# Kernel tuning notes

Hardware: AMD Instinct MI355X
Metric: run time of the kernel (lower is better)

## Reference

```python
import jax, jax.numpy as jnp
import numpy as np
import math

B, S, D = 16, 256, 1024   # batch, seq (= s_model), d_model
HP, HC = 16, 8
DK, SK = D // HP, S // HC
EPS = 1e-6


def setup_inputs() -> dict:
    key = jax.random.key(0)
    ks = jax.random.split(key, 3)
    x = jax.random.normal(ks[0], (B, S, D), dtype=jnp.float32)
    Wp = jax.random.normal(ks[1], (3, D, D), dtype=jnp.float32) * 0.02  # (in,out)
    bp = jnp.zeros((3, D), dtype=jnp.float32)
    Wc = jax.random.normal(ks[2], (4, S, S), dtype=jnp.float32) * 0.02  # (in,out)
    bc = jnp.zeros((4, S), dtype=jnp.float32)
    a_p = jnp.ones((D,), dtype=jnp.float32)
    b_p = jnp.zeros((D,), dtype=jnp.float32)
    a_c = jnp.ones((S,), dtype=jnp.float32)
    b_c = jnp.zeros((S,), dtype=jnp.float32)
    return {"x": x, "Wp": Wp, "bp": bp, "Wc": Wc, "bc": bc,
            "a_p": a_p, "b_p": b_p, "a_c": a_c, "b_c": b_c}


def _std(x, axis):
    # torch .std(): unbiased (ddof=1)
    return jnp.std(x, axis=axis, keepdims=True, ddof=1)


def _attn(q, k, v):
    # q,k,v: [B, H, T, dk]; dropout is identity (eval)
    scores = jnp.einsum('bhtd,bhsd->bhts', q, k) / math.sqrt(q.shape[-1])
    p = jax.nn.softmax(scores, axis=-1)
    return jnp.einsum('bhts,bhsd->bhtd', p, v)


def reference(x, Wp, bp, Wc, bc, a_p, b_p, a_c, b_c):
    nb = x.shape[0]
    # ---- LayerNorm over channels (norm_p) ----
    mean = jnp.mean(x, axis=-1, keepdims=True)
    xp = a_p * (x - mean) / (_std(x, -1) + EPS) + b_p            # [B,S,D]
    # ---- positional attention over sequence ----
    qkv = jnp.einsum('bsd,nde->nbse', xp, Wp) + bp[:, None, None, :]
    q, k, v = [t.reshape(nb, S, HP, DK).transpose(0, 2, 1, 3) for t in qkv]
    xp = _attn(q, k, v).transpose(0, 2, 1, 3).reshape(nb, S, D)  # [B,S,D]
    # ---- LayerNorm_C: stats over sequence dim, affine indexed by seq ----
    mean_c = jnp.mean(xp, axis=-2, keepdims=True)                # [B,1,D]
    xc = a_c[:, None] * (xp - mean_c) / (_std(xp, -2) + EPS) + b_c[:, None]
    # ---- channel attention: channels are tokens, head dim SK ----
    xt = xc.transpose(0, 2, 1)                                    # [B,D,S]
    qkvc = jnp.einsum('bds,nse->nbde', xt, Wc[:3]) + bc[:3, None, None, :]
    qc, kc, vc = [t.reshape(nb, D, HC, SK).transpose(0, 2, 1, 3) for t in qkvc]
    xcatt = _attn(qc, kc, vc).transpose(0, 2, 1, 3).reshape(nb, D, S)  # [B,D,S]
    out = jnp.einsum('bds,se->bde', xcatt, Wc[3]) + bc[3]         # [B,D,S]
    return out.transpose(0, 2, 1)                                  # [B,S,D]
```

## Files before the change

kernel.cpp:

```cpp
#include <hip/hip_runtime.h>
#include <hip/hip_bf16.h>
#include <math.h>

#define B_ 16
#define S_ 256
#define D_ 1024
#define HP_ 16
#define DK_ 64
#define HC_ 8
#define SK_ 32
#define EPS_ 1e-6f

#define ALPHA_P 0.42466089973135876f
#define ALPHA_C 0.50500991942f

typedef __attribute__((ext_vector_type(8))) short short8v;
typedef __attribute__((ext_vector_type(4))) float f32x4;

__device__ __forceinline__ float bf2f(unsigned short h) {
    return __uint_as_float((unsigned)h << 16);
}
__device__ __forceinline__ ushort2 f2bf2(float a, float b) {
    __hip_bfloat162 h = __float22bfloat162_rn(make_float2(a, b));
    union { __hip_bfloat162 h2; ushort2 u2; } cv;
    cv.h2 = h;
    return cv.u2;
}
__device__ __forceinline__ float exp2_fast(float x) {
    float r;
    asm("v_exp_f32 %0, %1\n\ts_nop 0" : "=v"(r) : "v"(x));
    return r;
}
__device__ __forceinline__ void ldlds16(const unsigned short* g, unsigned short* l) {
    const unsigned int* gp = reinterpret_cast<const unsigned int*>(g);
    auto* lp = reinterpret_cast<__attribute__((address_space(3))) unsigned int*>(
        reinterpret_cast<uintptr_t>(l));
    __builtin_amdgcn_global_load_lds(gp, lp, 16, 0, 0);
}

__global__ __launch_bounds__(256) void k1_ln_p(
    const float* __restrict__ x, const float* __restrict__ a_p,
    const float* __restrict__ b_p, unsigned short* __restrict__ xh,
    unsigned short* __restrict__ xl)
{
    const int row = blockIdx.x;
    const float4* xr = (const float4*)(x + (size_t)row * D_);
    const int tid = threadIdx.x;
    float4 v = xr[tid];
    float s  = v.x + v.y + v.z + v.w;
    float sq = v.x*v.x + v.y*v.y + v.z*v.z + v.w*v.w;
    #pragma unroll
    for (int off = 32; off > 0; off >>= 1) {
        s  += __shfl_down(s, off);
        sq += __shfl_down(sq, off);
    }
    __shared__ float red[8];
    const int wid = tid >> 6, lane = tid & 63;
    if (lane == 0) { red[wid] = s; red[4 + wid] = sq; }
    __syncthreads();
    if (tid == 0) {
        float S0 = red[0] + red[1] + red[2] + red[3];
        float Q0 = red[4] + red[5] + red[6] + red[7];
        float mean = S0 / (float)D_;
        float var  = fmaxf((Q0 - (float)D_ * mean * mean) / (float)(D_ - 1), 0.0f);
        red[0] = mean;
        red[1] = 1.0f / (sqrtf(var) + EPS_);
    }
    __syncthreads();
    const float mean = red[0], inv = red[1];
    float4 a = ((const float4*)a_p)[tid];
    float4 b = ((const float4*)b_p)[tid];
    float o0 = a.x * (v.x - mean) * inv + b.x;
    float o1 = a.y * (v.y - mean) * inv + b.y;
    float o2 = a.z * (v.z - mean) * inv + b.z;
    float o3 = a.w * (v.w - mean) * inv + b.w;
    ushort2 h01 = f2bf2(o0, o1), h23 = f2bf2(o2, o3);
    ushort2 l01 = f2bf2(o0 - bf2f(h01.x), o1 - bf2f(h01.y));
    ushort2 l23 = f2bf2(o2 - bf2f(h23.x), o3 - bf2f(h23.y));
    ushort4 hv, lv;
    hv.x = h01.x; hv.y = h01.y; hv.z = h23.x; hv.w = h23.y;
    lv.x = l01.x; lv.y = l01.y; lv.z = l23.x; lv.w = l23.y;
    *(ushort4*)&xh[(size_t)row * D_ + tid*4] = hv;
    *(ushort4*)&xl[(size_t)row * D_ + tid*4] = lv;
}

__global__ __launch_bounds__(256) void tsplit(
    const float* __restrict__ W, unsigned short* __restrict__ Th,
    unsigned short* __restrict__ Tl, int K, int N)
{
    const int z = blockIdx.z;
    W  += (size_t)z * K * N;
    Th += (size_t)z * K * N;
    Tl += (size_t)z * K * N;
    const int k0 = blockIdx.x * 64, n0 = blockIdx.y * 64;
    __shared__ float tile[64][65];
    const int ix = threadIdx.x & 63, iy = threadIdx.x >> 6;
    #pragma unroll
    for (int u = 0; u < 16; u++) {
        const int kk = iy*16 + u;
        tile[kk][ix] = W[(size_t)(k0+kk)*N + n0 + ix];
    }
    __syncthreads();
    #pragma unroll
    for (int u = 0; u < 16; u += 2) {
        const int nn0 = iy*16 + u, nn1 = nn0 + 1;
        const float v0 = tile[ix][nn0], v1 = tile[ix][nn1];
        ushort2 h2 = f2bf2(v0, v1);
        ushort2 l2 = f2bf2(v0 - bf2f(h2.x), v1 - bf2f(h2.y));
        Th[(size_t)(n0+nn0)*K + k0 + ix] = h2.x;
        Th[(size_t)(n0+nn1)*K + k0 + ix] = h2.y;
        Tl[(size_t)(n0+nn0)*K + k0 + ix] = l2.x;
        Tl[(size_t)(n0+nn1)*K + k0 + ix] = l2.y;
    }
}

template<int OUTMODE>
__global__ __launch_bounds__(256) void mm_mfma(
    const unsigned short* __restrict__ Ah, const unsigned short* __restrict__ Al,
    const unsigned short* __restrict__ Bh, const unsigned short* __restrict__ Bl,
    const float* __restrict__ bias, void* __restrict__ Cout1,
    void* __restrict__ Cout2,
    int M, int N, int K, long sB, long sBias, long sC, long loff, int TB,
    float alpha, int zsplit, int zobase, int lognx)
{
    const int nwg = gridDim.x * gridDim.y * gridDim.z;
    const int chunk = nwg >> 3;
    const int flat = blockIdx.x + gridDim.x * (blockIdx.y + gridDim.y * blockIdx.z);
    const int logical = (flat & 7) * chunk + (flat >> 3);
    const int bz  = logical >> 8;
    const int rem = logical & 255;
    const int bx  = rem & ((1 << lognx) - 1);
    const int by  = rem >> lognx;
    const int zeff = bz + zobase;
    Bh   += (size_t)bz * sB;
    Bl   += (size_t)bz * sB;
    bias += (size_t)zeff * sBias;
    const int n0 = bx * 128, m0 = by * 128;
    __shared__ __align__(16) unsigned short Ash[2][128*32], Als[2][128*32];
    __shared__ __align__(16) unsigned short Bsh[2][128*32], Bls[2][128*32];
    const int tid = threadIdx.x;
    const int wave = tid >> 6, lane = tid & 63;
    const int wm = wave & 1, wn = wave >> 1;
    const int lrow = lane & 15, quad = lane >> 4;
    size_t gaOff[2], gbOff[2];
    int cb[2];
    #pragma unroll
    for (int j = 0; j < 2; j++) {
        const int p = wave*128 + j*64 + lane;
        const int row = p >> 2;
        const int cc = (p & 3) ^ ((row >> 1) & 3);
        gaOff[j] = (size_t)(m0 + row) * K + cc*8;
        gbOff[j] = (size_t)(n0 + row) * K + cc*8;
        cb[j] = (wave*128 + j*64) * 8;
    }
    int aFr[4], bFr[4];
    #pragma unroll
    for (int i = 0; i < 4; i++) {
        const int ra = wm*64 + i*16 + lrow;
        aFr[i] = ((ra << 2) | (quad ^ ((ra >> 1) & 3))) * 8;
        const int rb = wn*64 + i*16 + lrow;
        bFr[i] = ((rb << 2) | (quad ^ ((rb >> 1) & 3))) * 8;
    }
    f32x4 acc[4][4];
    #pragma unroll
    for (int j = 0; j < 4; j++) {
        const float bv = bias[n0 + wn*64 + j*16 + lrow];
        #pragma unroll
        for (int i = 0; i < 4; i++) {
            acc[i][j][0] = bv; acc[i][j][1] = bv; acc[i][j][2] = bv; acc[i][j][3] = bv;
        }
    }
    #pragma unroll
    for (int j = 0; j < 2; j++) {
        ldlds16(Ah + gaOff[j], &Ash[0][cb[j]]);
        ldlds16(Al + gaOff[j], &Als[0][cb[j]]);
        ldlds16(Bh + gbOff[j], &Bsh[0][cb[j]]);
        ldlds16(Bl + gbOff[j], &Bls[0][cb[j]]);
    }
    const int NT = K >> 5;
    for (int kt = 0; kt < NT; kt++) {
        const int cur = kt & 1;
        asm volatile("s_waitcnt vmcnt(0)" ::: "memory");
        asm volatile("s_barrier" ::: "memory");
        if (kt + 1 < NT) {
            const int kk = (kt + 1) * 32;
            #pragma unroll
            for (int j = 0; j < 2; j++) {
                ldlds16(Ah + gaOff[j] + kk, &Ash[cur^1][cb[j]]);
                ldlds16(Al + gaOff[j] + kk, &Als[cur^1][cb[j]]);
                ldlds16(Bh + gbOff[j] + kk, &Bsh[cur^1][cb[j]]);
                ldlds16(Bl + gbOff[j] + kk, &Bls[cur^1][cb[j]]);
            }
        }
        short8v bhf[4], blf[4];
        #pragma unroll
        for (int j = 0; j < 4; j++) {
            bhf[j] = *(const short8v*)&Bsh[cur][bFr[j]];
            blf[j] = *(const short8v*)&Bls[cur][bFr[j]];
        }
        #pragma unroll
        for (int i = 0; i < 4; i++) {
            short8v ahf = *(const short8v*)&Ash[cur][aFr[i]];
            short8v alf = *(const short8v*)&Als[cur][aFr[i]];
            #pragma unroll
            for (int j = 0; j < 4; j++) {
                acc[i][j] = __builtin_amdgcn_mfma_f32_16x16x32_bf16(ahf, bhf[j], acc[i][j], 0, 0, 0);
                acc[i][j] = __builtin_amdgcn_mfma_f32_16x16x32_bf16(ahf, blf[j], acc[i][j], 0, 0, 0);
                acc[i][j] = __builtin_amdgcn_mfma_f32_16x16x32_bf16(alf, bhf[j], acc[i][j], 0, 0, 0);
            }
        }
    }
    #pragma unroll
    for (int i = 0; i < 4; i++) {
        const int mrow = m0 + wm*64 + i*16 + quad*4;
        #pragma unroll
        for (int j = 0; j < 4; j++) {
            const int ncol = n0 + wn*64 + j*16 + lrow;
            if (OUTMODE == 1) {
                if (zeff < zsplit) {
                    unsigned short* Ch = (unsigned short*)Cout1 + (size_t)zeff * sC;
                    unsigned short* Cl = Ch + loff;
                    #pragma unroll
                    for (int r = 0; r < 4; r += 2) {
                        const float v0 = acc[i][j][r] * alpha;
                        const float v1 = acc[i][j][r+1] * alpha;
                        ushort2 h2 = f2bf2(v0, v1);
                        ushort2 l2 = f2bf2(v0 - bf2f(h2.x), v1 - bf2f(h2.y));
                        Ch[(size_t)(mrow + r    ) * N + ncol] = h2.x;
                        Ch[(size_t)(mrow + r + 1) * N + ncol] = h2.y;
                        Cl[(size_t)(mrow + r    ) * N + ncol] = l2.x;
                        Cl[(size_t)(mrow + r + 1) * N + ncol] = l2.y;
                    }
                } else {
                    unsigned short* Ch = (unsigned short*)Cout2;
                    unsigned short* Cl = Ch + loff;
                    const int bidx = mrow / TB, t0 = mrow % TB;
                    const size_t ad = (size_t)bidx * N * TB + (size_t)ncol * TB + t0;
                    const float v0 = acc[i][j][0], v1 = acc[i][j][1];
                    const float v2 = acc[i][j][2], v3 = acc[i][j][3];
                    ushort2 h01 = f2bf2(v0, v1), h23 = f2bf2(v2, v3);
                    ushort2 l01 = f2bf2(v0 - bf2f(h01.x), v1 - bf2f(h01.y));
                    ushort2 l23 = f2bf2(v2 - bf2f(h23.x), v3 - bf2f(h23.y));
                    ushort4 hv, lv;
                    hv.x = h01.x; hv.y = h01.y; hv.z = h23.x; hv.w = h23.y;
                    lv.x = l01.x; lv.y = l01.y; lv.z = l23.x; lv.w = l23.y;
                    *(ushort4*)&Ch[ad] = hv;
                    *(ushort4*)&Cl[ad] = lv;
                }
            } else {
                float* C = (float*)Cout2;
                const int bidx = mrow / TB, t0 = mrow % TB;
                f32x4 a4 = acc[i][j];
                *(float4*)&C[((size_t)bidx * N + ncol) * TB + t0] = *(float4*)&a4;
            }
        }
    }
}

__global__ __launch_bounds__(256) void k3_mfma(
    const unsigned short* __restrict__ qh, const unsigned short* __restrict__ ql,
    const unsigned short* __restrict__ kh, const unsigned short* __restrict__ kl,
    const unsigned short* __restrict__ vth, const unsigned short* __restrict__ vtl,
    float* __restrict__ out)
{
    const int flat = blockIdx.x + (blockIdx.y << 2) + (blockIdx.z << 6);
    const int logical = ((flat & 7) << 7) | (flat >> 3);
    const int m0 = (logical & 3) * 64;
    const int h  = (logical >> 2) & 15;
    const int b  = logical >> 6;
    const int hoff = h * DK_;
    const size_t rowb = (size_t)b * S_;
    __shared__ __align__(16) unsigned short Ksh[2][64*64], Ksl[2][64*64];
    __shared__ __align__(16) unsigned short VTh[2][64*64], VTl[2][64*64];
    __shared__ __align__(16) unsigned short Ps[64][72];
    const int tid = threadIdx.x;
    const int w = tid >> 6, lane = tid & 63;
    const int lrow = lane & 15, quad = lane >> 4;
    short8v bqh[2], bql[2];
    #pragma unroll
    for (int ks = 0; ks < 2; ks++) {
        const size_t qb = (rowb + m0 + w*16 + lrow) * D_ + hoff + ks*32 + quad*8;
        bqh[ks] = *(const short8v*)&qh[qb];
        bql[ks] = *(const short8v*)&ql[qb];
    }
    size_t kOff[2], vOff[2];
    int cb[2];
    #pragma unroll
    for (int j = 0; j < 2; j++) {
        const int p = w*128 + j*64 + lane;
        const int row = p >> 3;
        const int cc = (p & 7) ^ (row & 7);
        kOff[j] = (rowb + row) * D_ + hoff + cc*8;
        vOff[j] = ((size_t)b * D_ + hoff + row) * S_ + cc*8;
        cb[j] = (w*128 + j*64) * 8;
    }
    f32x4 o[4] = {};
    float lacc = 0.f;
    #pragma unroll
    for (int j = 0; j < 2; j++) {
        ldlds16(kh  + kOff[j], &Ksh[0][cb[j]]);
        ldlds16(kl  + kOff[j], &Ksl[0][cb[j]]);
        ldlds16(vth + vOff[j], &VTh[0][cb[j]]);
        ldlds16(vtl + vOff[j], &VTl[0][cb[j]]);
    }
    for (int kt = 0; kt < 4; kt++) {
        const int cur = kt & 1;
        asm volatile("s_waitcnt vmcnt(0)" ::: "memory");
        asm volatile("s_barrier" ::: "memory");
        if (kt < 3) {
            const int n01 = (kt + 1) * 64;
            #pragma unroll
            for (int j = 0; j < 2; j++) {
                ldlds16(kh  + kOff[j] + (size_t)n01 * D_, &Ksh[cur^1][cb[j]]);
                ldlds16(kl  + kOff[j] + (size_t)n01 * D_, &Ksl[cur^1][cb[j]]);
                ldlds16(vth + vOff[j] + n01,              &VTh[cur^1][cb[j]]);
                ldlds16(vtl + vOff[j] + n01,              &VTl[cur^1][cb[j]]);
            }
        }
        f32x4 sa[4] = {};
        #pragma unroll
        for (int ks = 0; ks < 2; ks++) {
            #pragma unroll
            for (int jk = 0; jk < 4; jk++) {
                const int r = jk*16 + lrow, c = ks*4 + quad;
                const int off = ((r << 3) | (c ^ (r & 7))) * 8;
                short8v akh = *(const short8v*)&Ksh[cur][off];
                short8v akl = *(const short8v*)&Ksl[cur][off];
                sa[jk] = __builtin_amdgcn_mfma_f32_16x16x32_bf16(akh, bqh[ks], sa[jk], 0, 0, 0);
                sa[jk] = __builtin_amdgcn_mfma_f32_16x16x32_bf16(akl, bqh[ks], sa[jk], 0, 0, 0);
                sa[jk] = __builtin_amdgcn_mfma_f32_16x16x32_bf16(akh, bql[ks], sa[jk], 0, 0, 0);
            }
        }
        #pragma unroll
        for (int jk = 0; jk < 4; jk++) {
            float p0 = exp2_fast(sa[jk][0]);
            float p1 = exp2_fast(sa[jk][1]);
            float p2 = exp2_fast(sa[jk][2]);
            float p3 = exp2_fast(sa[jk][3]);
            lacc += (p0 + p1) + (p2 + p3);
            ushort2 p01 = f2bf2(p0, p1), p23 = f2bf2(p2, p3);
            ushort4 ph;
            ph.x = p01.x; ph.y = p01.y; ph.z = p23.x; ph.w = p23.y;
            *(ushort4*)&Ps[w*16 + lrow][jk*16 + quad*4] = ph;
        }
        #pragma unroll
        for (int ks = 0; ks < 2; ks++) {
            short8v ap = *(const short8v*)&Ps[w*16 + lrow][ks*32 + quad*8];
            #pragma unroll
            for (int nf = 0; nf < 4; nf++) {
                const int r = nf*16 + lrow, c = ks*4 + quad;
                const int off = ((r << 3) | (c ^ (r & 7))) * 8;
                short8v vH = *(const short8v*)&VTh[cur][off];
                short8v vL = *(const short8v*)&VTl[cur][off];
                o[nf] = __builtin_amdgcn_mfma_f32_16x16x32_bf16(ap, vH, o[nf], 0, 0, 0);
                o[nf] = __builtin_amdgcn_mfma_f32_16x16x32_bf16(ap, vL, o[nf], 0, 0, 0);
            }
        }
    }
    lacc += __shfl_xor(lacc, 16);
    lacc += __shfl_xor(lacc, 32);
    #pragma unroll
    for (int r = 0; r < 4; r++) {
        const float linv = 1.0f / __shfl(lacc, quad*4 + r);
        #pragma unroll
        for (int nf = 0; nf < 4; nf++)
            out[(rowb + m0 + w*16 + quad*4 + r) * D_ + hoff + nf*16 + lrow] =
                o[nf][r] * linv;
    }
}

__global__ __launch_bounds__(256) void k6_mfma(
    const unsigned short* __restrict__ qch, const unsigned short* __restrict__ qcl,
    const unsigned short* __restrict__ kch, const unsigned short* __restrict__ kcl,
    const unsigned short* __restrict__ vth, const unsigned short* __restrict__ vtl,
    unsigned short* __restrict__ oh, unsigned short* __restrict__ ol)
{
    const int flat = blockIdx.x + (blockIdx.y << 3) + (blockIdx.z << 6);
    const int logical = ((flat & 7) << 7) | (flat >> 3);
    const int m0 = (logical & 7) << 7;
    const int h  = (logical >> 3) & 7;
    const int b  = logical >> 6;
    const int hoff = h * SK_;
    const size_t rowb = (size_t)b * D_;
    __shared__ __align__(16) unsigned short Ksh[2][64*32], Ksl[2][64*32];
    __shared__ __align__(16) unsigned short VTh[2][32*64], VTl[2][32*64];
    __shared__ __align__(16) unsigned short Ps[128][72];
    const int tid = threadIdx.x;
    const int w = tid >> 6, lane = tid & 63;
    const int lrow = lane & 15, quad = lane >> 4;
    short8v bqh[2], bql[2];
    #pragma unroll
    for (int i = 0; i < 2; i++) {
        const size_t qb = (rowb + m0 + w*32 + i*16 + lrow) * S_ + hoff + quad*8;
        bqh[i] = *(const short8v*)&qch[qb];
        bql[i] = *(const short8v*)&qcl[qb];
    }
    size_t kOff, vOff;
    {
        const int pK = w*64 + lane;
        const int rowK = pK >> 2;
        const int ccK = (pK & 3) ^ ((rowK >> 1) & 3);
        kOff = (rowb + rowK) * S_ + hoff + ccK*8;
        const int pV = w*64 + lane;
        const int rowV = pV >> 3;
        const int ccV = (pV & 7) ^ (rowV & 7);
        vOff = ((size_t)b * S_ + hoff + rowV) * D_ + ccV*8;
    }
    const int cb = w*64*8;
    f32x4 o[2][2] = {};
    float lacc[2] = {0.f, 0.f};
    ldlds16(kch + kOff, &Ksh[0][cb]);
    ldlds16(kcl + kOff, &Ksl[0][cb]);
    ldlds16(vth + vOff, &VTh[0][cb]);
    ldlds16(vtl + vOff, &VTl[0][cb]);
    for (int kt = 0; kt < 16; kt++) {
        const int cur = kt & 1;
        asm volatile("s_waitcnt vmcnt(0)" ::: "memory");
        asm volatile("s_barrier" ::: "memory");
        if (kt < 15) {
            const int n01 = (kt + 1) * 64;
            ldlds16(kch + kOff + (size_t)n01 * S_, &Ksh[cur^1][cb]);
            ldlds16(kcl + kOff + (size_t)n01 * S_, &Ksl[cur^1][cb]);
            ldlds16(vth + vOff + n01,              &VTh[cur^1][cb]);
            ldlds16(vtl + vOff + n01,              &VTl[cur^1][cb]);
        }
        f32x4 sa[2][4] = {};
        #pragma unroll
        for (int jk = 0; jk < 4; jk++) {
            const int r = jk*16 + lrow;
            const int off = ((r << 2) | (quad ^ ((r >> 1) & 3))) * 8;
            short8v akh = *(const short8v*)&Ksh[cur][off];
            short8v akl = *(const short8v*)&Ksl[cur][off];
            #pragma unroll
            for (int i = 0; i < 2; i++) {
                sa[i][jk] = __builtin_amdgcn_mfma_f32_16x16x32_bf16(akh, bqh[i], sa[i][jk], 0, 0, 0);
                sa[i][jk] = __builtin_amdgcn_mfma_f32_16x16x32_bf16(akl, bqh[i], sa[i][jk], 0, 0, 0);
                sa[i][jk] = __builtin_amdgcn_mfma_f32_16x16x32_bf16(akh, bql[i], sa[i][jk], 0, 0, 0);
            }
        }
        #pragma unroll
        for (int i = 0; i < 2; i++)
            #pragma unroll
            for (int jk = 0; jk < 4; jk++) {
                float p0 = exp2_fast(sa[i][jk][0]);
                float p1 = exp2_fast(sa[i][jk][1]);
                float p2 = exp2_fast(sa[i][jk][2]);
                float p3 = exp2_fast(sa[i][jk][3]);
                lacc[i] += (p0 + p1) + (p2 + p3);
                ushort2 p01 = f2bf2(p0, p1), p23 = f2bf2(p2, p3);
                ushort4 ph;
                ph.x = p01.x; ph.y = p01.y; ph.z = p23.x; ph.w = p23.y;
                *(ushort4*)&Ps[w*32 + i*16 + lrow][jk*16 + quad*4] = ph;
            }
        #pragma unroll
        for (int ks = 0; ks < 2; ks++) {
            short8v ap[2];
            #pragma unroll
            for (int i = 0; i < 2; i++)
                ap[i] = *(const short8v*)&Ps[w*32 + i*16 + lrow][ks*32 + quad*8];
            #pragma unroll
            for (int nf = 0; nf < 2; nf++) {
                const int r = nf*16 + lrow, c = ks*4 + quad;
                const int off = ((r << 3) | (c ^ (r & 7))) * 8;
                short8v vHf = *(const short8v*)&VTh[cur][off];
                short8v vLf = *(const short8v*)&VTl[cur][off];
                #pragma unroll
                for (int i = 0; i < 2; i++) {
                    o[i][nf] = __builtin_amdgcn_mfma_f32_16x16x32_bf16(ap[i], vHf, o[i][nf], 0, 0, 0);
                    o[i][nf] = __builtin_amdgcn_mfma_f32_16x16x32_bf16(ap[i], vLf, o[i][nf], 0, 0, 0);
                }
            }
        }
    }
    #pragma unroll
    for (int i = 0; i < 2; i++) {
        lacc[i] += __shfl_xor(lacc[i], 16);
        lacc[i] += __shfl_xor(lacc[i], 32);
    }
    #pragma unroll
    for (int i = 0; i < 2; i++)
        #pragma unroll
        for (int r = 0; r < 4; r++) {
            const float linv = 1.0f / __shfl(lacc[i], quad*4 + r);
            const float v0 = o[i][0][r] * linv;
            const float v1 = o[i][1][r] * linv;
            ushort2 h2 = f2bf2(v0, v1);
            ushort2 l2 = f2bf2(v0 - bf2f(h2.x), v1 - bf2f(h2.y));
            const size_t idx =
                (rowb + m0 + w*32 + i*16 + quad*4 + r) * S_ + hoff + lrow;
            oh[idx]      = h2.x;
            oh[idx + 16] = h2.y;
            ol[idx]      = l2.x;
            ol[idx + 16] = l2.y;
        }
}

__global__ __launch_bounds__(256) void k4_fused(
    const float* __restrict__ x, const float* __restrict__ a_c,
    const float* __restrict__ b_c, unsigned short* __restrict__ xth,
    unsigned short* __restrict__ xtl)
{
    const int d0 = blockIdx.x * 64, b = blockIdx.y;
    __shared__ float tile[256][65];
    __shared__ float part[8][64];
    __shared__ float stats[2][64];
    __shared__ float acs[256], bcs[256];
    const int tid = threadIdx.x;
    acs[tid] = a_c[tid];
    bcs[tid] = b_c[tid];
    const int dl = tid & 63, sq = tid >> 6;
    float s1 = 0.f, s2 = 0.f;
    #pragma unroll 8
    for (int u = 0; u < 64; u++) {
        const int srow = sq*64 + u;
        const float v = x[((size_t)(b*S_ + srow))*D_ + d0 + dl];
        tile[srow][dl] = v;
        s1 += v; s2 += v*v;
    }
    part[sq][dl] = s1; part[4+sq][dl] = s2;
    __syncthreads();
    if (tid < 64) {
        const float S = part[0][tid]+part[1][tid]+part[2][tid]+part[3][tid];
        const float Q = part[4][tid]+part[5][tid]+part[6][tid]+part[7][tid];
        const float mean = S / (float)S_;
        const float var  = fmaxf((Q - (float)S_*mean*mean)/(float)(S_-1), 0.f);
        stats[0][tid] = mean;
        stats[1][tid] = 1.f/(sqrtf(var)+EPS_);
    }
    __syncthreads();
    const int dd = tid >> 2, s00 = (tid & 3) * 64;
    const float mean = stats[0][dd], inv = stats[1][dd];
    const size_t obase = ((size_t)(b*D_ + d0 + dd))*S_ + s00;
    #pragma unroll
    for (int c = 0; c < 8; c++) {
        union { ushort u[8]; uint4 v4; } hb, lb;
        #pragma unroll
        for (int t = 0; t < 8; t += 2) {
            const int s = s00 + c*8 + t;
            const float v0 = acs[s]  *(tile[s][dd]  -mean)*inv + bcs[s];
            const float v1 = acs[s+1]*(tile[s+1][dd]-mean)*inv + bcs[s+1];
            ushort2 h2 = f2bf2(v0, v1);
            ushort2 l2 = f2bf2(v0 - bf2f(h2.x), v1 - bf2f(h2.y));
            hb.u[t] = h2.x; hb.u[t+1] = h2.y;
            lb.u[t] = l2.x; lb.u[t+1] = l2.y;
        }
        *(uint4*)&xth[obase + c*8] = hb.v4;
        *(uint4*)&xtl[obase + c*8] = lb.v4;
    }
}

extern "C" void kernel_launch(void* const* d_in, const int* in_sizes, int n_in,
                              void* d_out, int out_size, void* d_ws, size_t ws_size,
                              hipStream_t stream)
{
    const float* x   = (const float*)d_in[0];
    const float* Wp  = (const float*)d_in[1];
    const float* bp  = (const float*)d_in[2];
    const float* Wc  = (const float*)d_in[3];
    const float* bc  = (const float*)d_in[4];
    const float* a_p = (const float*)d_in[5];
    const float* b_p = (const float*)d_in[6];
    const float* a_c = (const float*)d_in[7];
    const float* b_c = (const float*)d_in[8];
    float* out = (float*)d_out;
    float* ws  = (float*)d_ws;
    const size_t NE = (size_t)B_ * S_ * D_;

    float* S0 = ws;
    float* S1 = ws + NE;
    float* S2 = ws + 2*NE;
    float* S3 = ws + 3*NE;
    unsigned short* SW = (unsigned short*)(ws + 4*NE);

    const size_t baseBytes = 4*NE*sizeof(float);
    const bool big = ws_size >= baseBytes + (size_t)2 * 3 * D_ * D_ * sizeof(unsigned short) * 2;

    unsigned short* xh = (unsigned short*)S0;
    unsigned short* xl = xh + NE;
    unsigned short* q_h  = (unsigned short*)S1;
    unsigned short* k_h  = (unsigned short*)S2;
    unsigned short* vt_h = (unsigned short*)S3;

    k1_ln_p<<<dim3(B_*S_), 256, 0, stream>>>(x, a_p, b_p, xh, xl);

    if (big) {
        unsigned short* WTh = SW;
        unsigned short* WTl = WTh + (size_t)3 * D_ * D_;
        tsplit<<<dim3(D_/64, D_/64, 3), 256, 0, stream>>>(Wp, WTh, WTl, D_, D_);
        mm_mfma<1><<<dim3(D_/128, (B_*S_)/128, 3), 256, 0, stream>>>(
            xh, xl, WTh, WTl, bp, (void*)q_h, (void*)vt_h,
            B_*S_, D_, D_, (long)D_*D_, (long)D_, (long)(2*NE), (long)NE, S_,
            ALPHA_P, 2, 0, 3);
    } else {
        unsigned short* WTh = SW;
        unsigned short* WTl = WTh + (size_t)D_ * D_;
        for (int z = 0; z < 3; z++) {
            tsplit<<<dim3(D_/64, D_/64, 1), 256, 0, stream>>>(
                Wp + (size_t)z*D_*D_, WTh, WTl, D_, D_);
            mm_mfma<1><<<dim3(D_/128, (B_*S_)/128, 1), 256, 0, stream>>>(
                xh, xl, WTh, WTl, bp, (void*)q_h, (void*)vt_h,
                B_*S_, D_, D_, 0, (long)D_, (long)(2*NE), (long)NE, S_,
                ALPHA_P, 2, z, 3);
        }
    }

    k3_mfma<<<dim3(S_/64, HP_, B_), 256, 0, stream>>>(
        q_h, q_h + NE, k_h, k_h + NE, vt_h, vt_h + NE, S0);

    unsigned short* xth = (unsigned short*)S1;
    k4_fused<<<dim3(D_/64, B_), 256, 0, stream>>>(S0, a_c, b_c, xth, xth + NE);

    unsigned short* WcTh = SW;
    unsigned short* WcTl = WcTh + (size_t)4 * S_ * S_;
    tsplit<<<dim3(S_/64, S_/64, 4), 256, 0, stream>>>(Wc, WcTh, WcTl, S_, S_);
    unsigned short* qc_h  = (unsigned short*)S2;
    unsigned short* vct_h = (unsigned short*)S0;
    mm_mfma<1><<<dim3(S_/128, (B_*D_)/128, 3), 256, 0, stream>>>(
        xth, xth + NE, WcTh, WcTl, bc, (void*)qc_h, (void*)vct_h,
        B_*D_, S_, S_, (long)S_*S_, (long)S_, (long)(2*NE), (long)NE, D_,
        ALPHA_C, 2, 0, 1);

    unsigned short* kc_h = (unsigned short*)S3;
    unsigned short* xch  = (unsigned short*)S1;
    k6_mfma<<<dim3(D_/128, HC_, B_), 256, 0, stream>>>(
        qc_h, qc_h + NE, kc_h, kc_h + NE, vct_h, vct_h + NE, xch, xch + NE);

    mm_mfma<3><<<dim3(S_/128, (B_*D_)/128, 1), 256, 0, stream>>>(
        xch, xch + NE, WcTh + (size_t)3*S_*S_, WcTl + (size_t)3*S_*S_, bc + 3*S_,
        nullptr, (void*)out, B_*D_, S_, S_, 0, 0, 0, 0, D_, 1.0f, 0, 0, 1);
}
```

Baseline: 317.4 us.

## Fuse Q/K/V projections into one GEMM block sharing A tiles

```diff
diff --git a/kernel.cpp b/kernel.cpp
--- a/kernel.cpp
+++ b/kernel.cpp
@@ -114,7 +114,7 @@
     }
 }
 
-template<int OUTMODE>
+template<int OUTMODE, int Z>
 __global__ __launch_bounds__(256) void mm_mfma(
     const unsigned short* __restrict__ Ah, const unsigned short* __restrict__ Al,
     const unsigned short* __restrict__ Bh, const unsigned short* __restrict__ Bl,
@@ -123,21 +123,15 @@
     int M, int N, int K, long sB, long sBias, long sC, long loff, int TB,
     float alpha, int zsplit, int zobase, int lognx)
 {
-    const int nwg = gridDim.x * gridDim.y * gridDim.z;
+    const int nwg = gridDim.x * gridDim.y;
     const int chunk = nwg >> 3;
-    const int flat = blockIdx.x + gridDim.x * (blockIdx.y + gridDim.y * blockIdx.z);
+    const int flat = blockIdx.x + gridDim.x * blockIdx.y;
     const int logical = (flat & 7) * chunk + (flat >> 3);
-    const int bz  = logical >> 8;
-    const int rem = logical & 255;
-    const int bx  = rem & ((1 << lognx) - 1);
-    const int by  = rem >> lognx;
-    const int zeff = bz + zobase;
-    Bh   += (size_t)bz * sB;
-    Bl   += (size_t)bz * sB;
-    bias += (size_t)zeff * sBias;
+    const int bx = logical & ((1 << lognx) - 1);
+    const int by = logical >> lognx;
     const int n0 = bx * 128, m0 = by * 128;
-    __shared__ __align__(16) unsigned short Ash[2][128*32], Als[2][128*32];
-    __shared__ __align__(16) unsigned short Bsh[2][128*32], Bls[2][128*32];
+    __shared__ __align__(16) unsigned short Ash[2][2][128*32];
+    __shared__ __align__(16) unsigned short Bsh[2][Z][2][128*32];
     const int tid = threadIdx.x;
     const int wave = tid >> 6, lane = tid & 63;
     const int wm = wave & 1, wn = wave >> 1;
@@ -161,21 +155,27 @@
         const int rb = wn*64 + i*16 + lrow;
         bFr[i] = ((rb << 2) | (quad ^ ((rb >> 1) & 3))) * 8;
     }
-    f32x4 acc[4][4];
-    #pragma unroll
-    for (int j = 0; j < 4; j++) {
-        const float bv = bias[n0 + wn*64 + j*16 + lrow];
-        #pragma unroll
-        for (int i = 0; i < 4; i++) {
-            acc[i][j][0] = bv; acc[i][j][1] = bv; acc[i][j][2] = bv; acc[i][j][3] = bv;
-        }
-    }
+    f32x4 acc[Z][4][4];
+    #pragma unroll
+    for (int z = 0; z < Z; z++)
+        #pragma unroll
+        for (int j = 0; j < 4; j++) {
+            const float bv = bias[(size_t)(z + zobase) * sBias + n0 + wn*64 + j*16 + lrow];
+            #pragma unroll
+            for (int i = 0; i < 4; i++) {
+                acc[z][i][j][0] = bv; acc[z][i][j][1] = bv;
+                acc[z][i][j][2] = bv; acc[z][i][j][3] = bv;
+            }
+        }
     #pragma unroll
     for (int j = 0; j < 2; j++) {
-        ldlds16(Ah + gaOff[j], &Ash[0][cb[j]]);
-        ldlds16(Al + gaOff[j], &Als[0][cb[j]]);
-        ldlds16(Bh + gbOff[j], &Bsh[0][cb[j]]);
-        ldlds16(Bl + gbOff[j], &Bls[0][cb[j]]);
+        ldlds16(Ah + gaOff[j], &Ash[0][0][cb[j]]);
+        ldlds16(Al + gaOff[j], &Ash[0][1][cb[j]]);
+        #pragma unroll
+        for (int z = 0; z < Z; z++) {
+            ldlds16(Bh + (size_t)z * sB + gbOff[j], &Bsh[0][z][0][cb[j]]);
+            ldlds16(Bl + (size_t)z * sB + gbOff[j], &Bsh[0][z][1][cb[j]]);
+        }
     }
     const int NT = K >> 5;
     for (int kt = 0; kt < NT; kt++) {
@@ -186,72 +186,86 @@
             const int kk = (kt + 1) * 32;
             #pragma unroll
             for (int j = 0; j < 2; j++) {
-                ldlds16(Ah + gaOff[j] + kk, &Ash[cur^1][cb[j]]);
-                ldlds16(Al + gaOff[j] + kk, &Als[cur^1][cb[j]]);
-                ldlds16(Bh + gbOff[j] + kk, &Bsh[cur^1][cb[j]]);
-                ldlds16(Bl + gbOff[j] + kk, &Bls[cur^1][cb[j]]);
-            }
-        }
-        short8v bhf[4], blf[4];
-        #pragma unroll
-        for (int j = 0; j < 4; j++) {
-            bhf[j] = *(const short8v*)&Bsh[cur][bFr[j]];
-            blf[j] = *(const short8v*)&Bls[cur][bFr[j]];
-        }
+                ldlds16(Ah + gaOff[j] + kk, &Ash[cur^1][0][cb[j]]);
+                ldlds16(Al + gaOff[j] + kk, &Ash[cur^1][1][cb[j]]);
+                #pragma unroll
+                for (int z = 0; z < Z; z++) {
+                    ldlds16(Bh + (size_t)z * sB + gbOff[j] + kk, &Bsh[cur^1][z][0][cb[j]]);
+                    ldlds16(Bl + (size_t)z * sB + gbOff[j] + kk, &Bsh[cur^1][z][1][cb[j]]);
+                }
+            }
+        }
+        short8v ahf[4], alf[4];
         #pragma unroll
         for (int i = 0; i < 4; i++) {
-            short8v ahf = *(const short8v*)&Ash[cur][aFr[i]];
-            short8v alf = *(const short8v*)&Als[cur][aFr[i]];
+            ahf[i] = *(const short8v*)&Ash[cur][0][aFr[i]];
+            alf[i] = *(const short8v*)&Ash[cur][1][aFr[i]];
+        }
+        #pragma unroll
+        for (int z = 0; z < Z; z++) {
+            short8v bhf[4], blf[4];
             #pragma unroll
             for (int j = 0; j < 4; j++) {
-                acc[i][j] = __builtin_amdgcn_mfma_f32_16x16x32_bf16(ahf, bhf[j], acc[i][j], 0, 0, 0);
-                acc[i][j] = __builtin_amdgcn_mfma_f32_16x16x32_bf16(ahf, blf[j], acc[i][j], 0, 0, 0);
-                acc[i][j] = __builtin_amdgcn_mfma_f32_16x16x32_bf16(alf, bhf[j], acc[i][j], 0, 0, 0);
-            }
-        }
-    }
-    #pragma unroll
-    for (int i = 0; i < 4; i++) {
-        const int mrow = m0 + wm*64 + i*16 + quad*4;
-        #pragma unroll
-        for (int j = 0; j < 4; j++) {
-            const int ncol = n0 + wn*64 + j*16 + lrow;
-            if (OUTMODE == 1) {
-                if (zeff < zsplit) {
-                    unsigned short* Ch = (unsigned short*)Cout1 + (size_t)zeff * sC;
-                    unsigned short* Cl = Ch + loff;
-                    #pragma unroll
-                    for (int r = 0; r < 4; r += 2) {
-                        const float v0 = acc[i][j][r] * alpha;
-                        const float v1 = acc[i][j][r+1] * alpha;
-                        ushort2 h2 = f2bf2(v0, v1);
-                        ushort2 l2 = f2bf2(v0 - bf2f(h2.x), v1 - bf2f(h2.y));
-                        Ch[(size_t)(mrow + r    ) * N + ncol] = h2.x;
-                        Ch[(size_t)(mrow + r + 1) * N + ncol] = h2.y;
-                        Cl[(size_t)(mrow + r    ) * N + ncol] = l2.x;
-                        Cl[(size_t)(mrow + r + 1) * N + ncol] = l2.y;
+                bhf[j] = *(const short8v*)&Bsh[cur][z][0][bFr[j]];
+                blf[j] = *(const short8v*)&Bsh[cur][z][1][bFr[j]];
+            }
+            #pragma unroll
+            for (int i = 0; i < 4; i++) {
+                #pragma unroll
+                for (int j = 0; j < 4; j++) {
+                    acc[z][i][j] = __builtin_amdgcn_mfma_f32_16x16x32_bf16(ahf[i], bhf[j], acc[z][i][j], 0, 0, 0);
+                    acc[z][i][j] = __builtin_amdgcn_mfma_f32_16x16x32_bf16(ahf[i], blf[j], acc[z][i][j], 0, 0, 0);
+                    acc[z][i][j] = __builtin_amdgcn_mfma_f32_16x16x32_bf16(alf[i], bhf[j], acc[z][i][j], 0, 0, 0);
+                }
+            }
+        }
+    }
+    #pragma unroll
+    for (int z = 0; z < Z; z++) {
+        const int zeff = z + zobase;
+        #pragma unroll
+        for (int i = 0; i < 4; i++) {
+            const int mrow = m0 + wm*64 + i*16 + quad*4;
+            #pragma unroll
+            for (int j = 0; j < 4; j++) {
+                const int ncol = n0 + wn*64 + j*16 + lrow;
+                if (OUTMODE == 1) {
+                    if (zeff < zsplit) {
+                        unsigned short* Ch = (unsigned short*)Cout1 + (size_t)zeff * sC;
+                        unsigned short* Cl = Ch + loff;
+                        #pragma unroll
+                        for (int r = 0; r < 4; r += 2) {
+                            const float v0 = acc[z][i][j][r] * alpha;
+                            const float v1 = acc[z][i][j][r+1] * alpha;
+                            ushort2 h2 = f2bf2(v0, v1);
+                            ushort2 l2 = f2bf2(v0 - bf2f(h2.x), v1 - bf2f(h2.y));
+                            Ch[(size_t)(mrow + r    ) * N + ncol] = h2.x;
+                            Ch[(size_t)(mrow + r + 1) * N + ncol] = h2.y;
+                            Cl[(size_t)(mrow + r    ) * N + ncol] = l2.x;
+                            Cl[(size_t)(mrow + r + 1) * N + ncol] = l2.y;
+                        }
+                    } else {
+                        unsigned short* Ch = (unsigned short*)Cout2;
+                        unsigned short* Cl = Ch + loff;
+                        const int bidx = mrow / TB, t0 = mrow % TB;
+                        const size_t ad = (size_t)bidx * N * TB + (size_t)ncol * TB + t0;
+                        const float v0 = acc[z][i][j][0], v1 = acc[z][i][j][1];
+                        const float v2 = acc[z][i][j][2], v3 = acc[z][i][j][3];
+                        ushort2 h01 = f2bf2(v0, v1), h23 = f2bf2(v2, v3);
+                        ushort2 l01 = f2bf2(v0 - bf2f(h01.x), v1 - bf2f(h01.y));
+                        ushort2 l23 = f2bf2(v2 - bf2f(h23.x), v3 - bf2f(h23.y));
+                        ushort4 hv, lv;
+                        hv.x = h01.x; hv.y = h01.y; hv.z = h23.x; hv.w = h23.y;
+                        lv.x = l01.x; lv.y = l01.y; lv.z = l23.x; lv.w = l23.y;
+                        *(ushort4*)&Ch[ad] = hv;
+                        *(ushort4*)&Cl[ad] = lv;
                     }
                 } else {
-                    unsigned short* Ch = (unsigned short*)Cout2;
-                    unsigned short* Cl = Ch + loff;
+                    float* C = (float*)Cout2;
                     const int bidx = mrow / TB, t0 = mrow % TB;
-                    const size_t ad = (size_t)bidx * N * TB + (size_t)ncol * TB + t0;
-                    const float v0 = acc[i][j][0], v1 = acc[i][j][1];
-                    const float v2 = acc[i][j][2], v3 = acc[i][j][3];
-                    ushort2 h01 = f2bf2(v0, v1), h23 = f2bf2(v2, v3);
-                    ushort2 l01 = f2bf2(v0 - bf2f(h01.x), v1 - bf2f(h01.y));
-                    ushort2 l23 = f2bf2(v2 - bf2f(h23.x), v3 - bf2f(h23.y));
-                    ushort4 hv, lv;
-                    hv.x = h01.x; hv.y = h01.y; hv.z = h23.x; hv.w = h23.y;
-                    lv.x = l01.x; lv.y = l01.y; lv.z = l23.x; lv.w = l23.y;
-                    *(ushort4*)&Ch[ad] = hv;
-                    *(ushort4*)&Cl[ad] = lv;
+                    f32x4 a4 = acc[z][i][j];
+                    *(float4*)&C[((size_t)bidx * N + ncol) * TB + t0] = *(float4*)&a4;
                 }
-            } else {
-                float* C = (float*)Cout2;
-                const int bidx = mrow / TB, t0 = mrow % TB;
-                f32x4 a4 = acc[i][j];
-                *(float4*)&C[((size_t)bidx * N + ncol) * TB + t0] = *(float4*)&a4;
             }
         }
     }
@@ -587,7 +601,7 @@
         unsigned short* WTh = SW;
         unsigned short* WTl = WTh + (size_t)3 * D_ * D_;
         tsplit<<<dim3(D_/64, D_/64, 3), 256, 0, stream>>>(Wp, WTh, WTl, D_, D_);
-        mm_mfma<1><<<dim3(D_/128, (B_*S_)/128, 3), 256, 0, stream>>>(
+        mm_mfma<1,3><<<dim3(D_/128, (B_*S_)/128), 256, 0, stream>>>(
             xh, xl, WTh, WTl, bp, (void*)q_h, (void*)vt_h,
             B_*S_, D_, D_, (long)D_*D_, (long)D_, (long)(2*NE), (long)NE, S_,
             ALPHA_P, 2, 0, 3);
@@ -597,7 +611,7 @@
         for (int z = 0; z < 3; z++) {
             tsplit<<<dim3(D_/64, D_/64, 1), 256, 0, stream>>>(
                 Wp + (size_t)z*D_*D_, WTh, WTl, D_, D_);
-            mm_mfma<1><<<dim3(D_/128, (B_*S_)/128, 1), 256, 0, stream>>>(
+            mm_mfma<1,1><<<dim3(D_/128, (B_*S_)/128), 256, 0, stream>>>(
                 xh, xl, WTh, WTl, bp, (void*)q_h, (void*)vt_h,
                 B_*S_, D_, D_, 0, (long)D_, (long)(2*NE), (long)NE, S_,
                 ALPHA_P, 2, z, 3);
@@ -615,7 +629,7 @@
     tsplit<<<dim3(S_/64, S_/64, 4), 256, 0, stream>>>(Wc, WcTh, WcTl, S_, S_);
     unsigned short* qc_h  = (unsigned short*)S2;
     unsigned short* vct_h = (unsigned short*)S0;
-    mm_mfma<1><<<dim3(S_/128, (B_*D_)/128, 3), 256, 0, stream>>>(
+    mm_mfma<1,3><<<dim3(S_/128, (B_*D_)/128), 256, 0, stream>>>(
         xth, xth + NE, WcTh, WcTl, bc, (void*)qc_h, (void*)vct_h,
         B_*D_, S_, S_, (long)S_*S_, (long)S_, (long)(2*NE), (long)NE, D_,
         ALPHA_C, 2, 0, 1);
@@ -625,7 +639,7 @@
     k6_mfma<<<dim3(D_/128, HC_, B_), 256, 0, stream>>>(
         qc_h, qc_h + NE, kc_h, kc_h + NE, vct_h, vct_h + NE, xch, xch + NE);
 
-    mm_mfma<3><<<dim3(S_/128, (B_*D_)/128, 1), 256, 0, stream>>>(
+    mm_mfma<3,1><<<dim3(S_/128, (B_*D_)/128), 256, 0, stream>>>(
         xch, xch + NE, WcTh + (size_t)3*S_*S_, WcTl + (size_t)3*S_*S_, bc + 3*S_,
         nullptr, (void*)out, B_*D_, S_, S_, 0, 0, 0, 0, D_, 1.0f, 0, 0, 1);
 }
```

Result: faster. 307.0 us (-3.3%).

## Replace GEMM with 512-thread 256x128 tile kernel using triple-buffered LDS ring

Applied to the files above, without the earlier changes.

```diff
diff --git a/kernel.cpp b/kernel.cpp
--- a/kernel.cpp
+++ b/kernel.cpp
@@ -114,8 +114,27 @@
     }
 }
 
+#define MF3(i, j, ah, al)                                                          \
+    acc[i][j] = __builtin_amdgcn_mfma_f32_16x16x32_bf16(ah, bhf[j], acc[i][j], 0, 0, 0); \
+    acc[i][j] = __builtin_amdgcn_mfma_f32_16x16x32_bf16(ah, blf[j], acc[i][j], 0, 0, 0); \
+    acc[i][j] = __builtin_amdgcn_mfma_f32_16x16x32_bf16(al, bhf[j], acc[i][j], 0, 0, 0);
+
+#define PHASE(p, ISSUE)                                                            \
+    {                                                                              \
+        short8v ah_ = *(const short8v*)&Ash[cur][0][aFr[p]];                       \
+        short8v al_ = *(const short8v*)&Ash[cur][1][aFr[p]];                       \
+        ISSUE                                                                      \
+        __builtin_amdgcn_s_barrier();                                              \
+        asm volatile("s_waitcnt lgkmcnt(0)" ::: "memory");                         \
+        __builtin_amdgcn_sched_barrier(0);                                         \
+        __builtin_amdgcn_s_setprio(1);                                             \
+        MF3(p, 0, ah_, al_) MF3(p, 1, ah_, al_)                                    \
+        MF3(p, 2, ah_, al_) MF3(p, 3, ah_, al_)                                    \
+        __builtin_amdgcn_s_setprio(0);                                             \
+    }
+
 template<int OUTMODE>
-__global__ __launch_bounds__(256) void mm_mfma(
+__global__ __launch_bounds__(512, 2) void mm_ring(
     const unsigned short* __restrict__ Ah, const unsigned short* __restrict__ Al,
     const unsigned short* __restrict__ Bh, const unsigned short* __restrict__ Bl,
     const float* __restrict__ bias, void* __restrict__ Cout1,
@@ -123,35 +142,42 @@
     int M, int N, int K, long sB, long sBias, long sC, long loff, int TB,
     float alpha, int zsplit, int zobase, int lognx)
 {
-    const int nwg = gridDim.x * gridDim.y * gridDim.z;
+    const int nwg = gridDim.x * gridDim.y;
     const int chunk = nwg >> 3;
-    const int flat = blockIdx.x + gridDim.x * (blockIdx.y + gridDim.y * blockIdx.z);
+    const int flat = blockIdx.x + gridDim.x * blockIdx.y;
     const int logical = (flat & 7) * chunk + (flat >> 3);
-    const int bz  = logical >> 8;
-    const int rem = logical & 255;
+    const int bz  = logical >> 7;
+    const int rem = logical & 127;
     const int bx  = rem & ((1 << lognx) - 1);
     const int by  = rem >> lognx;
     const int zeff = bz + zobase;
     Bh   += (size_t)bz * sB;
     Bl   += (size_t)bz * sB;
     bias += (size_t)zeff * sBias;
-    const int n0 = bx * 128, m0 = by * 128;
-    __shared__ __align__(16) unsigned short Ash[2][128*32], Als[2][128*32];
-    __shared__ __align__(16) unsigned short Bsh[2][128*32], Bls[2][128*32];
+    const int n0 = bx * 128, m0 = by * 256;
+    __shared__ __align__(16) unsigned short Ash[3][2][256*32];
+    __shared__ __align__(16) unsigned short Bsh[3][2][128*32];
     const int tid = threadIdx.x;
     const int wave = tid >> 6, lane = tid & 63;
-    const int wm = wave & 1, wn = wave >> 1;
+    const int wm = wave & 3, wn = wave >> 2;
     const int lrow = lane & 15, quad = lane >> 4;
-    size_t gaOff[2], gbOff[2];
-    int cb[2];
+    size_t gaOff[2];
+    int cbA[2];
     #pragma unroll
     for (int j = 0; j < 2; j++) {
-        const int p = wave*128 + j*64 + lane;
+        const int p = j*512 + tid;
         const int row = p >> 2;
         const int cc = (p & 3) ^ ((row >> 1) & 3);
         gaOff[j] = (size_t)(m0 + row) * K + cc*8;
-        gbOff[j] = (size_t)(n0 + row) * K + cc*8;
-        cb[j] = (wave*128 + j*64) * 8;
+        cbA[j] = (j*512 + wave*64) * 8;
+    }
+    size_t gbOff;
+    int cbB;
+    {
+        const int row = tid >> 2;
+        const int cc = (tid & 3) ^ ((row >> 1) & 3);
+        gbOff = (size_t)(n0 + row) * K + cc*8;
+        cbB = (wave*64) * 8;
     }
     int aFr[4], bFr[4];
     #pragma unroll
@@ -170,46 +196,56 @@
             acc[i][j][0] = bv; acc[i][j][1] = bv; acc[i][j][2] = bv; acc[i][j][3] = bv;
         }
     }
-    #pragma unroll
-    for (int j = 0; j < 2; j++) {
-        ldlds16(Ah + gaOff[j], &Ash[0][cb[j]]);
-        ldlds16(Al + gaOff[j], &Als[0][cb[j]]);
-        ldlds16(Bh + gbOff[j], &Bsh[0][cb[j]]);
-        ldlds16(Bl + gbOff[j], &Bls[0][cb[j]]);
-    }
+    #define STAGE6(t, buf)                                           \
+        {                                                            \
+            const int kk_ = (t) * 32;                                \
+            ldlds16(Bh + gbOff     + kk_, &Bsh[buf][0][cbB]);        \
+            ldlds16(Bl + gbOff     + kk_, &Bsh[buf][1][cbB]);        \
+            ldlds16(Ah + gaOff[0]  + kk_, &Ash[buf][0][cbA[0]]);     \
+            ldlds16(Al + gaOff[0]  + kk_, &Ash[buf][1][cbA[0]]);     \
+            ldlds16(Ah + gaOff[1]  + kk_, &Ash[buf][0][cbA[1]]);     \
+            ldlds16(Al + gaOff[1]  + kk_, &Ash[buf][1][cbA[1]]);     \
+        }
     const int NT = K >> 5;
+    STAGE6(0, 0)
+    STAGE6(1, 1)
+    int cur = 0;
     for (int kt = 0; kt < NT; kt++) {
-        const int cur = kt & 1;
-        asm volatile("s_waitcnt vmcnt(0)" ::: "memory");
-        asm volatile("s_barrier" ::: "memory");
-        if (kt + 1 < NT) {
-            const int kk = (kt + 1) * 32;
-            #pragma unroll
-            for (int j = 0; j < 2; j++) {
-                ldlds16(Ah + gaOff[j] + kk, &Ash[cur^1][cb[j]]);
-                ldlds16(Al + gaOff[j] + kk, &Als[cur^1][cb[j]]);
-                ldlds16(Bh + gbOff[j] + kk, &Bsh[cur^1][cb[j]]);
-                ldlds16(Bl + gbOff[j] + kk, &Bls[cur^1][cb[j]]);
-            }
-        }
+        if (kt == NT - 1) {
+            asm volatile("s_waitcnt vmcnt(0)" ::: "memory");
+        } else {
+            asm volatile("s_waitcnt vmcnt(6)" ::: "memory");
+        }
+        __builtin_amdgcn_s_barrier();
+        const int nx2 = (cur >= 1) ? cur - 1 : 2;
         short8v bhf[4], blf[4];
         #pragma unroll
         for (int j = 0; j < 4; j++) {
-            bhf[j] = *(const short8v*)&Bsh[cur][bFr[j]];
-            blf[j] = *(const short8v*)&Bls[cur][bFr[j]];
-        }
-        #pragma unroll
-        for (int i = 0; i < 4; i++) {
-            short8v ahf = *(const short8v*)&Ash[cur][aFr[i]];
-            short8v alf = *(const short8v*)&Als[cur][aFr[i]];
-            #pragma unroll
-            for (int j = 0; j < 4; j++) {
-                acc[i][j] = __builtin_amdgcn_mfma_f32_16x16x32_bf16(ahf, bhf[j], acc[i][j], 0, 0, 0);
-                acc[i][j] = __builtin_amdgcn_mfma_f32_16x16x32_bf16(ahf, blf[j], acc[i][j], 0, 0, 0);
-                acc[i][j] = __builtin_amdgcn_mfma_f32_16x16x32_bf16(alf, bhf[j], acc[i][j], 0, 0, 0);
-            }
-        }
-    }
+            bhf[j] = *(const short8v*)&Bsh[cur][0][bFr[j]];
+            blf[j] = *(const short8v*)&Bsh[cur][1][bFr[j]];
+        }
+        PHASE(0,
+            if (kt + 2 < NT) {
+                const int kk2 = (kt + 2) * 32;
+                ldlds16(Bh + gbOff + kk2, &Bsh[nx2][0][cbB]);
+                ldlds16(Bl + gbOff + kk2, &Bsh[nx2][1][cbB]);
+            })
+        PHASE(1,
+            if (kt + 2 < NT) {
+                const int kk2 = (kt + 2) * 32;
+                ldlds16(Ah + gaOff[0] + kk2, &Ash[nx2][0][cbA[0]]);
+                ldlds16(Al + gaOff[0] + kk2, &Ash[nx2][1][cbA[0]]);
+            })
+        PHASE(2,
+            if (kt + 2 < NT) {
+                const int kk2 = (kt + 2) * 32;
+                ldlds16(Ah + gaOff[1] + kk2, &Ash[nx2][0][cbA[1]]);
+                ldlds16(Al + gaOff[1] + kk2, &Ash[nx2][1][cbA[1]]);
+            })
+        PHASE(3, )
+        cur = (cur + 1 == 3) ? 0 : cur + 1;
+    }
+    #undef STAGE6
     #pragma unroll
     for (int i = 0; i < 4; i++) {
         const int mrow = m0 + wm*64 + i*16 + quad*4;
@@ -587,7 +623,7 @@
         unsigned short* WTh = SW;
         unsigned short* WTl = WTh + (size_t)3 * D_ * D_;
         tsplit<<<dim3(D_/64, D_/64, 3), 256, 0, stream>>>(Wp, WTh, WTl, D_, D_);
-        mm_mfma<1><<<dim3(D_/128, (B_*S_)/128, 3), 256, 0, stream>>>(
+        mm_ring<1><<<dim3(128, 3), 512, 0, stream>>>(
             xh, xl, WTh, WTl, bp, (void*)q_h, (void*)vt_h,
             B_*S_, D_, D_, (long)D_*D_, (long)D_, (long)(2*NE), (long)NE, S_,
             ALPHA_P, 2, 0, 3);
@@ -597,7 +633,7 @@
         for (int z = 0; z < 3; z++) {
             tsplit<<<dim3(D_/64, D_/64, 1), 256, 0, stream>>>(
                 Wp + (size_t)z*D_*D_, WTh, WTl, D_, D_);
-            mm_mfma<1><<<dim3(D_/128, (B_*S_)/128, 1), 256, 0, stream>>>(
+            mm_ring<1><<<dim3(128, 1), 512, 0, stream>>>(
                 xh, xl, WTh, WTl, bp, (void*)q_h, (void*)vt_h,
                 B_*S_, D_, D_, 0, (long)D_, (long)(2*NE), (long)NE, S_,
                 ALPHA_P, 2, z, 3);
@@ -615,7 +651,7 @@
     tsplit<<<dim3(S_/64, S_/64, 4), 256, 0, stream>>>(Wc, WcTh, WcTl, S_, S_);
     unsigned short* qc_h  = (unsigned short*)S2;
     unsigned short* vct_h = (unsigned short*)S0;
-    mm_mfma<1><<<dim3(S_/128, (B_*D_)/128, 3), 256, 0, stream>>>(
+    mm_ring<1><<<dim3(128, 3), 512, 0, stream>>>(
         xth, xth + NE, WcTh, WcTl, bc, (void*)qc_h, (void*)vct_h,
         B_*D_, S_, S_, (long)S_*S_, (long)S_, (long)(2*NE), (long)NE, D_,
         ALPHA_C, 2, 0, 1);
@@ -625,7 +661,7 @@
     k6_mfma<<<dim3(D_/128, HC_, B_), 256, 0, stream>>>(
         qc_h, qc_h + NE, kc_h, kc_h + NE, vct_h, vct_h + NE, xch, xch + NE);
 
-    mm_mfma<3><<<dim3(S_/128, (B_*D_)/128, 1), 256, 0, stream>>>(
+    mm_ring<3><<<dim3(128, 1), 512, 0, stream>>>(
         xch, xch + NE, WcTh + (size_t)3*S_*S_, WcTl + (size_t)3*S_*S_, bc + 3*S_,
         nullptr, (void*)out, B_*D_, S_, S_, 0, 0, 0, 0, D_, 1.0f, 0, 0, 1);
 }
```

New measurement: 324.8 us. +2.3%, slower.
